# Performance work log

Measured on AMD Instinct MI355X. Metric: run time of the kernel, lower is better.

## Reference

```python
import jax, jax.numpy as jnp
import numpy as np

D_MODEL = 1024
NUM_HEADS = 16
D_K = D_MODEL // NUM_HEADS
BATCH = 8
SEQ = 1024


def setup_inputs() -> dict:
    key = jax.random.key(0)
    ks = jax.random.split(key, 16)
    s = 1.0 / np.sqrt(D_MODEL)
    def lin(i):
        W = jax.random.uniform(ks[i], (D_MODEL, D_MODEL), jnp.float32, -s, s)
        b = jax.random.uniform(ks[i + 1], (D_MODEL,), jnp.float32, -s, s)
        return W, b
    Wq, bq = lin(0)
    Wk, bk = lin(2)
    Wv, bv = lin(4)
    Wg, bg = lin(6)
    Wbeta, bbeta = lin(8)
    Wo, bo = lin(10)
    X = jax.random.normal(ks[12], (BATCH, SEQ, D_MODEL), jnp.float32)
    Y = jax.random.normal(ks[13], (BATCH, SEQ, D_MODEL), jnp.float32)
    return dict(X=X, Y=Y, Wq=Wq, bq=bq, Wk=Wk, bk=bk, Wv=Wv, bv=bv,
                Wg=Wg, bg=bg, Wbeta=Wbeta, bbeta=bbeta, Wo=Wo, bo=bo)


def _split_heads(x):
    b, s, _ = x.shape
    return x.reshape(b, s, NUM_HEADS, D_K).transpose(0, 2, 1, 3)  # [b,h,s,d_k]


def _attend(q_in, kv_in, Wq, bq, Wk, bk, Wv, bv, Wg, bg, Wbeta, bbeta, Wo, bo):
    Q = _split_heads(q_in @ Wq + bq)
    K = _split_heads(kv_in @ Wk + bk)
    V = _split_heads(kv_in @ Wv + bv)
    scores = jnp.einsum('bhqd,bhkd->bhqk', Q, K) / jnp.sqrt(jnp.float32(D_K))
    attn = jax.nn.softmax(scores, axis=-1)
    ctx = jnp.einsum('bhqk,bhkd->bhqd', attn, V)
    b, h, s, d = ctx.shape
    ctx = ctx.transpose(0, 2, 1, 3).reshape(b, s, h * d)
    out = (ctx @ Wg + bg) * jnp.sqrt(jnp.float32(D_K)) + (ctx @ Wbeta + bbeta)
    return out @ Wo + bo


def reference(X, Y, Wq, bq, Wk, bk, Wv, bv, Wg, bg, Wbeta, bbeta, Wo, bo):
    params = (Wq, bq, Wk, bk, Wv, bv, Wg, bg, Wbeta, bbeta, Wo, bo)
    Y_new = _attend(X, Y, *params)   # pass 1: queries from X, keys/values from Y
    X_new = _attend(Y_new, X, *params)  # pass 2: queries from new Y, kv from original X
    return (X_new, Y_new)
```

## Files before the change

### kernel.cpp

```cpp
#include <hip/hip_runtime.h>

typedef unsigned short u16;
typedef __bf16 bf16x8 __attribute__((ext_vector_type(8)));
typedef float f32x4 __attribute__((ext_vector_type(4)));
typedef float f32x16 __attribute__((ext_vector_type(16)));
typedef u16 u16x4 __attribute__((ext_vector_type(4)));
typedef unsigned int u32x4v __attribute__((ext_vector_type(4)));

#define LOG2E_OVER_8 0.18033688011112043f

__device__ __forceinline__ u16 f2bf(float f) {
  union { float f; unsigned int u; } x{f};
  unsigned int r = (x.u + 0x7fffu + ((x.u >> 16) & 1u)) >> 16;
  return (u16)r;
}

__device__ __forceinline__ float bf2f(u16 v) {
  union { unsigned int u; float f; } x;
  x.u = ((unsigned int)v) << 16;
  return x.f;
}

__device__ __forceinline__ unsigned cvtpk(float a, float b) {
  unsigned r;
  asm("v_cvt_pk_bf16_f32 %0, %1, %2" : "=v"(r) : "v"(a), "v"(b));
  return r;
}

__device__ __forceinline__ void gld16(const void* g, void* l) {
  __builtin_amdgcn_global_load_lds((const __attribute__((address_space(1))) unsigned int*)g,
                                   (__attribute__((address_space(3))) unsigned int*)l,
                                   16, 0, 0);
}

__global__ void prep_w(const float* __restrict__ Wq, const float* __restrict__ Wk,
                       const float* __restrict__ Wv, const float* __restrict__ Wg,
                       const float* __restrict__ Wb, const float* __restrict__ Wo,
                       u16* __restrict__ Wqt, u16* __restrict__ Wkt, u16* __restrict__ Wvt,
                       u16* __restrict__ Wcn, u16* __restrict__ Wot)
{
  __shared__ float tile[32][33];
  const int m = blockIdx.z;
  const int nb = blockIdx.x * 32, kb = blockIdx.y * 32;
  const int tx = threadIdx.x, ty = threadIdx.y;
  const float* src = (m == 0) ? Wq : (m == 1) ? Wk : (m == 2) ? Wv : (m == 3) ? Wg : Wo;
  u16* dst = (m == 0) ? Wqt : (m == 1) ? Wkt : (m == 2) ? Wvt : (m == 3) ? Wcn : Wot;
#pragma unroll
  for (int i = 0; i < 4; ++i) {
    const int k = kb + ty + i * 8;
    float v = src[k * 1024 + nb + tx];
    if (m == 3) v = 8.0f * v + Wb[k * 1024 + nb + tx];
    if (m == 0) v *= LOG2E_OVER_8;
    if (m == 3) dst[k * 1024 + nb + tx] = f2bf(v);
    else        tile[ty + i * 8][tx] = v;
  }
  __syncthreads();
  if (m != 3) {
#pragma unroll
    for (int i = 0; i < 4; ++i) {
      const int r = ty + i * 8;
      dst[(nb + r) * 1024 + kb + tx] = f2bf(tile[tx][r]);
    }
  }
}

__global__ void prep_b(const float* __restrict__ bq, const float* __restrict__ bg,
                       const float* __restrict__ bb,
                       float* __restrict__ bqs, float* __restrict__ bcs)
{
  const int i = blockIdx.x * 256 + threadIdx.x;
  if (i < 1024) {
    bqs[i] = bq[i] * LOG2E_OVER_8;
    bcs[i] = 8.0f * bg[i] + bb[i];
  }
}

__global__ void cvt2_bf16(const float* __restrict__ in0, u16* __restrict__ out0,
                          const float* __restrict__ in1, u16* __restrict__ out1, int n)
{
  int i = (blockIdx.x * blockDim.x + threadIdx.x) * 4;
  const int stride = gridDim.x * blockDim.x * 4;
  for (; i < n; i += stride) {
    const float4 v0 = *reinterpret_cast<const float4*>(in0 + i);
    u16x4 o0;
    o0.x = f2bf(v0.x); o0.y = f2bf(v0.y); o0.z = f2bf(v0.z); o0.w = f2bf(v0.w);
    *reinterpret_cast<u16x4*>(out0 + i) = o0;
    const float4 v1 = *reinterpret_cast<const float4*>(in1 + i);
    u16x4 o1;
    o1.x = f2bf(v1.x); o1.y = f2bf(v1.y); o1.z = f2bf(v1.z); o1.w = f2bf(v1.w);
    *reinterpret_cast<u16x4*>(out1 + i) = o1;
  }
}

template<int EPI, int NB>
__device__ __forceinline__ void gemm_body(int bid0, u16* lA, u16* lB,
                                          const u16* __restrict__ A,
                                          const u16* __restrict__ Bt,
                                          const float* __restrict__ bias,
                                          u16* __restrict__ outb, float* __restrict__ outf)
{
  int bid = (bid0 & 7) * NB + (bid0 >> 3);
  const int row0 = (bid >> 3) * 128;
  const int col0 = (bid & 7) * 128;
  const int t = threadIdx.x;
  const int w = t >> 6, lane = t & 63;
  const int l15 = lane & 15, l4 = lane >> 4;
  const int wr = w >> 1, wc = w & 1;
  const int l7 = l15 & 7;

  const u16* gA[4];
  const u16* gB[4];
#pragma unroll
  for (int k2 = 0; k2 < 4; ++k2) {
    const int c = k2 * 256 + t;
    const int r = c >> 3;
    const int sc = ((c & 7) ^ (r & 7)) * 8;
    gA[k2] = A + (row0 + r) * 1024 + sc;
    gB[k2] = Bt + (col0 + r) * 1024 + sc;
  }

  f32x4 acc[4][4] = {};

  for (int kt = 0; kt < 1024; kt += 64) {
#pragma unroll
    for (int k2 = 0; k2 < 4; ++k2) {
      gld16(gA[k2] + kt, lA + (k2 * 256 + w * 64) * 8);
      gld16(gB[k2] + kt, lB + (k2 * 256 + w * 64) * 8);
    }
    __syncthreads();
    bf16x8 aF[4][2], bF[4][2];
#pragma unroll
    for (int m = 0; m < 4; ++m)
#pragma unroll
      for (int ks = 0; ks < 2; ++ks)
        aF[m][ks] = *reinterpret_cast<const bf16x8*>(
            &lA[(wr * 64 + m * 16 + l15) * 64 + ((ks * 4 + l4) ^ l7) * 8]);
#pragma unroll
    for (int n = 0; n < 4; ++n)
#pragma unroll
      for (int ks = 0; ks < 2; ++ks)
        bF[n][ks] = *reinterpret_cast<const bf16x8*>(
            &lB[(wc * 64 + n * 16 + l15) * 64 + ((ks * 4 + l4) ^ l7) * 8]);
#pragma unroll
    for (int m = 0; m < 4; ++m)
#pragma unroll
      for (int n = 0; n < 4; ++n) {
        acc[m][n] = __builtin_amdgcn_mfma_f32_16x16x32_bf16(aF[m][0], bF[n][0], acc[m][n], 0, 0, 0);
        acc[m][n] = __builtin_amdgcn_mfma_f32_16x16x32_bf16(aF[m][1], bF[n][1], acc[m][n], 0, 0, 0);
      }
    __syncthreads();
  }

  float bv[4];
#pragma unroll
  for (int n = 0; n < 4; ++n)
    bv[n] = (EPI == 4) ? 0.0f : bias[col0 + wc * 64 + n * 16 + l15];
#pragma unroll
  for (int m = 0; m < 4; ++m) {
#pragma unroll
    for (int n = 0; n < 4; ++n) {
      const int c = col0 + wc * 64 + n * 16 + l15;
#pragma unroll
      for (int j = 0; j < 4; ++j) {
        const int r = row0 + wr * 64 + m * 16 + l4 * 4 + j;
        const float v = acc[m][n][j] + bv[n];
        if constexpr (EPI == 0 || EPI == 4) {
          outb[r * 1024 + c] = f2bf(v);
        } else if constexpr (EPI == 1) {
          outf[r * 1024 + c] = v;
          outb[r * 1024 + c] = f2bf(v);
        } else if constexpr (EPI == 2) {
          const int bi = r >> 10, s = r & 1023;
          const int h = c >> 6, d = c & 63;
          outb[((bi * 16 + h) * 64 + d) * 1024 + s] = f2bf(v);
        } else {
          outf[r * 1024 + c] = v;
        }
      }
    }
  }
}

__device__ __forceinline__ void bias_body(int bb, const float* __restrict__ bcs,
                                          const u16* __restrict__ Wot,
                                          const float* __restrict__ bo,
                                          float* __restrict__ bco)
{
  const int t = threadIdx.x, w = t >> 6, l = t & 63;
  const int n = bb * 4 + w;
  const u16* row = Wot + n * 1024;
  float a = 0.f;
#pragma unroll
  for (int i = 0; i < 16; ++i) a += bcs[l + 64 * i] * bf2f(row[l + 64 * i]);
#pragma unroll
  for (int d = 1; d < 64; d <<= 1) a += __shfl_xor(a, d);
  if (l == 0) bco[n] = a + bo[n];
}

template<int EPI, int NB = 64>
__global__ __launch_bounds__(256, 2)
void gemm_k(const u16* __restrict__ A, const u16* __restrict__ Bt,
            const float* __restrict__ bias,
            u16* __restrict__ outb, float* __restrict__ outf)
{
  __shared__ u16 lA[128 * 64];
  __shared__ u16 lB[128 * 64];
  gemm_body<EPI, NB>((int)blockIdx.x, lA, lB, A, Bt, bias, outb, outf);
}

__global__ __launch_bounds__(256, 2)
void gemmp1_k(const u16* __restrict__ Xb, const u16* __restrict__ Yb,
              const u16* __restrict__ Wqt, const float* __restrict__ bqs,
              const u16* __restrict__ Wkt, const float* __restrict__ bk,
              const u16* __restrict__ Wvt, const float* __restrict__ bv,
              u16* __restrict__ Qb, u16* __restrict__ Kb, u16* __restrict__ Vt,
              const u16* __restrict__ Wot, const u16* __restrict__ Wcn,
              u16* __restrict__ Wcot,
              const float* __restrict__ bcs, const float* __restrict__ bo,
              float* __restrict__ bco)
{
  __shared__ u16 lA[128 * 64];
  __shared__ u16 lB[128 * 64];
  const int id = (int)blockIdx.x;
  if (id < 512)       gemm_body<0, 64>(id,        lA, lB, Xb, Wqt, bqs, Qb, nullptr);
  else if (id < 1024) gemm_body<0, 64>(id - 512,  lA, lB, Yb, Wkt, bk, Kb, nullptr);
  else if (id < 1536) gemm_body<2, 64>(id - 1024, lA, lB, Yb, Wvt, bv, Vt, nullptr);
  else if (id < 1600) gemm_body<4, 8>(id - 1536,  lA, lB, Wot, Wcn, nullptr, Wcot, nullptr);
  else                bias_body(id - 1600, bcs, Wot, bo, bco);
}

__global__ __launch_bounds__(256, 2)
void gemmp2_k(const u16* __restrict__ A0, const u16* __restrict__ B0,
              const float* __restrict__ c0, u16* __restrict__ o0,
              const u16* __restrict__ A1, const u16* __restrict__ B1,
              const float* __restrict__ c1, u16* __restrict__ o1,
              const u16* __restrict__ A2, const u16* __restrict__ B2,
              const float* __restrict__ c2, u16* __restrict__ o2)
{
  __shared__ u16 lA[128 * 64];
  __shared__ u16 lB[128 * 64];
  const int id = (int)blockIdx.x;
  if (id < 512)       gemm_body<0, 64>(id,        lA, lB, A0, B0, c0, o0, nullptr);
  else if (id < 1024) gemm_body<0, 64>(id - 512,  lA, lB, A1, B1, c1, o1, nullptr);
  else                gemm_body<2, 64>(id - 1024, lA, lB, A2, B2, c2, o2, nullptr);
}

__global__ __launch_bounds__(256, 4)
void attn_k(const u16* __restrict__ Q, const u16* __restrict__ K,
            const u16* __restrict__ Vt, u16* __restrict__ ctx)
{
  __shared__ u16 lK[2][64 * 64];
  __shared__ u16 lV[2][64 * 64];
  __shared__ float lsumI[4][32];
  const int id = (int)blockIdx.x;
  const int xcd = id & 7, o = id >> 3;
  const int pair = xcd * 16 + (o >> 3);
  const int qt = o & 7;
  const int b = pair >> 4, h = pair & 15;
  const int t = threadIdx.x, w = t >> 6, lane = t & 63;
  const int l31 = lane & 31, hi = lane >> 5;
  const int q0 = qt * 128 + w * 32;
  const u16* Qp = Q + (size_t)b * (1024 * 1024) + h * 64;
  const u16* Kp = K + (size_t)b * (1024 * 1024) + h * 64;
  const u16* Vp = Vt + (size_t)(b * 16 + h) * (64 * 1024);

  const int r0 = t >> 3;
  const int scA = ((t & 7) ^ (r0 & 7)) * 8;
  const int l7r = l31 & 7;

  bf16x8 bQ[4];
#pragma unroll
  for (int ks = 0; ks < 4; ++ks)
    bQ[ks] = *reinterpret_cast<const bf16x8*>(&Qp[(q0 + l31) * 1024 + ks * 16 + hi * 8]);

  f32x16 acc[2] = {};
  float lsum = 0.f;

  auto STAGE = [&](int buf, int kv) {
    gld16(Kp + (size_t)(kv + r0) * 1024 + scA,        &lK[buf][(w * 64) * 8]);
    gld16(Kp + (size_t)(kv + r0 + 32) * 1024 + scA,   &lK[buf][(256 + w * 64) * 8]);
    gld16(Vp + (size_t)r0 * 1024 + kv + scA,          &lV[buf][(w * 64) * 8]);
    gld16(Vp + (size_t)(r0 + 32) * 1024 + kv + scA,   &lV[buf][(256 + w * 64) * 8]);
  };

  STAGE(0, 0);
  __syncthreads();

  for (int it = 0; it < 16; ++it) {
    const int cur = it & 1;
    if (it + 1 < 16) STAGE(cur ^ 1, (it + 1) * 64);

    f32x16 sS[2] = {};
    __builtin_amdgcn_s_setprio(1);
#pragma unroll
    for (int tt = 0; tt < 2; ++tt) {
#pragma unroll
      for (int ks = 0; ks < 4; ++ks) {
        const bf16x8 aK = *reinterpret_cast<const bf16x8*>(
            &lK[cur][(tt * 32 + l31) * 64 + ((2 * ks + hi) ^ l7r) * 8]);
        sS[tt] = __builtin_amdgcn_mfma_f32_32x32x16_bf16(aK, bQ[ks], sS[tt], 0, 0, 0);
      }
    }
    __builtin_amdgcn_s_setprio(0);

    unsigned pa[2][2][4];
#pragma unroll
    for (int tt = 0; tt < 2; ++tt) {
      float p[16];
      float s0 = 0.f, s1 = 0.f, s2 = 0.f, s3 = 0.f;
#pragma unroll
      for (int r = 0; r < 16; r += 4) {
        p[r]     = __builtin_amdgcn_exp2f(sS[tt][r]);
        p[r + 1] = __builtin_amdgcn_exp2f(sS[tt][r + 1]);
        p[r + 2] = __builtin_amdgcn_exp2f(sS[tt][r + 2]);
        p[r + 3] = __builtin_amdgcn_exp2f(sS[tt][r + 3]);
        s0 += p[r]; s1 += p[r + 1]; s2 += p[r + 2]; s3 += p[r + 3];
      }
      lsum += (s0 + s1) + (s2 + s3);
      unsigned wv[8];
#pragma unroll
      for (int i = 0; i < 8; ++i) wv[i] = cvtpk(p[2 * i], p[2 * i + 1]);
#pragma unroll
      for (int c = 0; c < 2; ++c) {
        unsigned a0 = wv[4 * c + 0], b0 = wv[4 * c + 2];
        unsigned a1 = wv[4 * c + 1], b1 = wv[4 * c + 3];
        asm("v_permlane32_swap_b32 %0, %1" : "+v"(a0), "+v"(b0));
        asm("v_permlane32_swap_b32 %0, %1" : "+v"(a1), "+v"(b1));
        pa[tt][c][0] = a0;
        pa[tt][c][1] = a1;
        pa[tt][c][2] = b0;
        pa[tt][c][3] = b1;
      }
    }

    __builtin_amdgcn_s_setprio(1);
#pragma unroll
    for (int tt = 0; tt < 2; ++tt)
#pragma unroll
      for (int c = 0; c < 2; ++c) {
        u32x4v pw;
        pw.x = pa[tt][c][0]; pw.y = pa[tt][c][1];
        pw.z = pa[tt][c][2]; pw.w = pa[tt][c][3];
        const bf16x8 aP = __builtin_bit_cast(bf16x8, pw);
#pragma unroll
        for (int dt = 0; dt < 2; ++dt) {
          const bf16x8 bV = *reinterpret_cast<const bf16x8*>(
              &lV[cur][(dt * 32 + l31) * 64 + ((4 * tt + 2 * c + hi) ^ l7r) * 8]);
          acc[dt] = __builtin_amdgcn_mfma_f32_32x32x16_bf16(aP, bV, acc[dt], 0, 0, 0);
        }
      }
    __builtin_amdgcn_s_setprio(0);
    __syncthreads();
  }

  const float ltot = lsum + __shfl_xor(lsum, 32);
  if (hi == 0) lsumI[w][l31] = 1.0f / ltot;
  u16* Cp = ctx + (size_t)b * (1024 * 1024) + h * 64;
#pragma unroll
  for (int dt = 0; dt < 2; ++dt)
#pragma unroll
    for (int r = 0; r < 16; ++r) {
      const int q = (r & 3) + 8 * (r >> 2) + 4 * hi;
      const float inv = lsumI[w][q];
      Cp[(q0 + q) * 1024 + dt * 32 + l31] = f2bf(acc[dt][r] * inv);
    }
}

extern "C" void kernel_launch(void* const* d_in, const int* in_sizes, int n_in,
                              void* d_out, int out_size, void* d_ws, size_t ws_size,
                              hipStream_t stream)
{
  (void)in_sizes; (void)n_in; (void)out_size; (void)ws_size;
  const float* X  = (const float*)d_in[0];
  const float* Y  = (const float*)d_in[1];
  const float* Wq = (const float*)d_in[2];
  const float* bq = (const float*)d_in[3];
  const float* Wk = (const float*)d_in[4];
  const float* bk = (const float*)d_in[5];
  const float* Wv = (const float*)d_in[6];
  const float* bv = (const float*)d_in[7];
  const float* Wg = (const float*)d_in[8];
  const float* bg = (const float*)d_in[9];
  const float* Wb = (const float*)d_in[10];
  const float* bb = (const float*)d_in[11];
  const float* Wo = (const float*)d_in[12];
  const float* bo = (const float*)d_in[13];
  float* out = (float*)d_out;
  char* ws = (char*)d_ws;
  const size_t MB = 1024ull * 1024ull;

  u16* Wqt = (u16*)(ws + 0 * MB);
  u16* Wkt = (u16*)(ws + 2 * MB);
  u16* Wvt = (u16*)(ws + 4 * MB);
  u16* Wcn = (u16*)(ws + 6 * MB);
  u16* Wot = (u16*)(ws + 8 * MB);
  u16* Wcot = (u16*)(ws + 10 * MB);
  u16* Xb = (u16*)(ws + 12 * MB);
  u16* Yb = (u16*)(ws + 28 * MB);
  u16* Qb = (u16*)(ws + 44 * MB);
  u16* Kb = (u16*)(ws + 60 * MB);
  u16* Vt = (u16*)(ws + 76 * MB);
  u16* Cx = (u16*)(ws + 92 * MB);
  float* bqs = (float*)(ws + 108 * MB);
  float* bcs = (float*)(ws + 108 * MB + 4096);
  float* bco = (float*)(ws + 108 * MB + 8192);
  const int NEL = 8 * 1024 * 1024;

  prep_w<<<dim3(32, 32, 5), dim3(32, 8), 0, stream>>>(Wq, Wk, Wv, Wg, Wb, Wo,
                                                      Wqt, Wkt, Wvt, Wcn, Wot);
  prep_b<<<4, 256, 0, stream>>>(bq, bg, bb, bqs, bcs);
  cvt2_bf16<<<2048, 256, 0, stream>>>(X, Xb, Y, Yb, NEL);

  gemmp1_k<<<1856, 256, 0, stream>>>(Xb, Yb, Wqt, bqs, Wkt, bk, Wvt, bv,
                                     Qb, Kb, Vt, Wot, Wcn, Wcot, bcs, bo, bco);
  attn_k<<<1024, 256, 0, stream>>>(Qb, Kb, Vt, Cx);
  gemm_k<1><<<512, 256, 0, stream>>>(Cx, Wcot, bco, Yb, out + NEL);

  gemmp2_k<<<1536, 256, 0, stream>>>(Yb, Wqt, bqs, Qb,
                                     Xb, Wkt, bk, Kb,
                                     Xb, Wvt, bv, Vt);
  attn_k<<<1024, 256, 0, stream>>>(Qb, Kb, Vt, Cx);
  gemm_k<3><<<512, 256, 0, stream>>>(Cx, Wcot, bco, nullptr, out);
}
```

Before: 282.5 us.

## Fold output projection into pass-2 query weights so Q2 comes from context directly

Precomposes the combined output weight with Wq (and the matching bias) into a new weight Wcoqt, so the second pass's queries are computed directly from the pass-1 context in the same launch that writes Y_new. This removes the bf16 Y_new round trip and its dependent Q projection GEMM. The weight composition adds a small extra GEMM (1024^3) in prep and changes rounding, since the composed weight is stored in bf16. Pass-2 K/V projection moves to its own launch.

After: 306.7 us. +8.6%, slower.

```diff
diff --git a/kernel.cpp b/kernel.cpp
--- a/kernel.cpp
+++ b/kernel.cpp
@@ -181,20 +181,20 @@
   }
 }
 
-__device__ __forceinline__ void bias_body(int bb, const float* __restrict__ bcs,
-                                          const u16* __restrict__ Wot,
-                                          const float* __restrict__ bo,
-                                          float* __restrict__ bco)
+__device__ __forceinline__ void bias_body(int bb, const float* __restrict__ vec,
+                                          const u16* __restrict__ Wt,
+                                          const float* __restrict__ add,
+                                          float* __restrict__ outv)
 {
   const int t = threadIdx.x, w = t >> 6, l = t & 63;
   const int n = bb * 4 + w;
-  const u16* row = Wot + n * 1024;
+  const u16* row = Wt + n * 1024;
   float a = 0.f;
 #pragma unroll
-  for (int i = 0; i < 16; ++i) a += bcs[l + 64 * i] * bf2f(row[l + 64 * i]);
+  for (int i = 0; i < 16; ++i) a += vec[l + 64 * i] * bf2f(row[l + 64 * i]);
 #pragma unroll
   for (int d = 1; d < 64; d <<= 1) a += __shfl_xor(a, d);
-  if (l == 0) bco[n] = a + bo[n];
+  if (l == 0) outv[n] = a + add[n];
 }
 
 template<int EPI, int NB = 64>
@@ -215,7 +215,7 @@
               const u16* __restrict__ Wvt, const float* __restrict__ bv,
               u16* __restrict__ Qb, u16* __restrict__ Kb, u16* __restrict__ Vt,
               const u16* __restrict__ Wot, const u16* __restrict__ Wcn,
-              u16* __restrict__ Wcot,
+              u16* __restrict__ Wcot, u16* __restrict__ Wcon,
               const float* __restrict__ bcs, const float* __restrict__ bo,
               float* __restrict__ bco)
 {
@@ -226,23 +226,48 @@
   else if (id < 1024) gemm_body<0, 64>(id - 512,  lA, lB, Yb, Wkt, bk, Kb, nullptr);
   else if (id < 1536) gemm_body<2, 64>(id - 1024, lA, lB, Yb, Wvt, bv, Vt, nullptr);
   else if (id < 1600) gemm_body<4, 8>(id - 1536,  lA, lB, Wot, Wcn, nullptr, Wcot, nullptr);
-  else                bias_body(id - 1600, bcs, Wot, bo, bco);
+  else if (id < 1664) gemm_body<4, 8>(id - 1600,  lA, lB, Wcn, Wot, nullptr, Wcon, nullptr);
+  else                bias_body(id - 1664, bcs, Wot, bo, bco);
 }
 
 __global__ __launch_bounds__(256, 2)
-void gemmp2_k(const u16* __restrict__ A0, const u16* __restrict__ B0,
-              const float* __restrict__ c0, u16* __restrict__ o0,
-              const u16* __restrict__ A1, const u16* __restrict__ B1,
-              const float* __restrict__ c1, u16* __restrict__ o1,
-              const u16* __restrict__ A2, const u16* __restrict__ B2,
-              const float* __restrict__ c2, u16* __restrict__ o2)
+void wprep2_k(const u16* __restrict__ Wqt, const u16* __restrict__ Wcon,
+              u16* __restrict__ Wcoqt,
+              const float* __restrict__ bco, const float* __restrict__ bqs,
+              float* __restrict__ bcoq)
 {
   __shared__ u16 lA[128 * 64];
   __shared__ u16 lB[128 * 64];
   const int id = (int)blockIdx.x;
-  if (id < 512)       gemm_body<0, 64>(id,        lA, lB, A0, B0, c0, o0, nullptr);
-  else if (id < 1024) gemm_body<0, 64>(id - 512,  lA, lB, A1, B1, c1, o1, nullptr);
-  else                gemm_body<2, 64>(id - 1024, lA, lB, A2, B2, c2, o2, nullptr);
+  if (id < 64) gemm_body<4, 8>(id, lA, lB, Wqt, Wcon, nullptr, Wcoqt, nullptr);
+  else         bias_body(id - 64, bco, Wqt, bqs, bcoq);
+}
+
+__global__ __launch_bounds__(256, 2)
+void yq2_k(const u16* __restrict__ Cx, const u16* __restrict__ Wcot,
+           const float* __restrict__ bco, float* __restrict__ outY,
+           const u16* __restrict__ Wcoqt, const float* __restrict__ bcoq,
+           u16* __restrict__ Qb)
+{
+  __shared__ u16 lA[128 * 64];
+  __shared__ u16 lB[128 * 64];
+  const int id = (int)blockIdx.x;
+  if (id < 512) gemm_body<3, 64>(id,       lA, lB, Cx, Wcot, bco, nullptr, outY);
+  else          gemm_body<0, 64>(id - 512, lA, lB, Cx, Wcoqt, bcoq, Qb, nullptr);
+}
+
+__global__ __launch_bounds__(256, 2)
+void kv2_k(const u16* __restrict__ Xb,
+           const u16* __restrict__ Wkt, const float* __restrict__ bk,
+           u16* __restrict__ Kb,
+           const u16* __restrict__ Wvt, const float* __restrict__ bv,
+           u16* __restrict__ Vt)
+{
+  __shared__ u16 lA[128 * 64];
+  __shared__ u16 lB[128 * 64];
+  const int id = (int)blockIdx.x;
+  if (id < 512) gemm_body<0, 64>(id,       lA, lB, Xb, Wkt, bk, Kb, nullptr);
+  else          gemm_body<2, 64>(id - 512, lA, lB, Xb, Wvt, bv, Vt, nullptr);
 }
 
 __global__ __launch_bounds__(256, 4)
@@ -404,6 +429,9 @@
   float* bqs = (float*)(ws + 108 * MB);
   float* bcs = (float*)(ws + 108 * MB + 4096);
   float* bco = (float*)(ws + 108 * MB + 8192);
+  float* bcoq = (float*)(ws + 108 * MB + 12288);
+  u16* Wcon  = (u16*)(ws + 110 * MB);
+  u16* Wcoqt = (u16*)(ws + 112 * MB);
   const int NEL = 8 * 1024 * 1024;
 
   prep_w<<<dim3(32, 32, 5), dim3(32, 8), 0, stream>>>(Wq, Wk, Wv, Wg, Wb, Wo,
@@ -411,14 +439,15 @@
   prep_b<<<4, 256, 0, stream>>>(bq, bg, bb, bqs, bcs);
   cvt2_bf16<<<2048, 256, 0, stream>>>(X, Xb, Y, Yb, NEL);
 
-  gemmp1_k<<<1856, 256, 0, stream>>>(Xb, Yb, Wqt, bqs, Wkt, bk, Wvt, bv,
-                                     Qb, Kb, Vt, Wot, Wcn, Wcot, bcs, bo, bco);
+  gemmp1_k<<<1920, 256, 0, stream>>>(Xb, Yb, Wqt, bqs, Wkt, bk, Wvt, bv,
+                                     Qb, Kb, Vt, Wot, Wcn, Wcot, Wcon,
+                                     bcs, bo, bco);
+  wprep2_k<<<320, 256, 0, stream>>>(Wqt, Wcon, Wcoqt, bco, bqs, bcoq);
+
   attn_k<<<1024, 256, 0, stream>>>(Qb, Kb, Vt, Cx);
-  gemm_k<1><<<512, 256, 0, stream>>>(Cx, Wcot, bco, Yb, out + NEL);
-
-  gemmp2_k<<<1536, 256, 0, stream>>>(Yb, Wqt, bqs, Qb,
-                                     Xb, Wkt, bk, Kb,
-                                     Xb, Wvt, bv, Vt);
+  yq2_k<<<1024, 256, 0, stream>>>(Cx, Wcot, bco, out + NEL, Wcoqt, bcoq, Qb);
+
+  kv2_k<<<1024, 256, 0, stream>>>(Xb, Wkt, bk, Kb, Wvt, bv, Vt);
   attn_k<<<1024, 256, 0, stream>>>(Qb, Kb, Vt, Cx);
   gemm_k<3><<<512, 256, 0, stream>>>(Cx, Wcot, bco, nullptr, out);
 }
```
